# Kernel tuning notes

Measured on AMD Instinct MI355X. Metric: run time of the kernel, lower is better.

Reference implementation:

```python
import jax, jax.numpy as jnp
import numpy as np

D_MODEL = 1024
D_KV = 64
N_HEADS = 16
INNER = N_HEADS * D_KV
EPS = 1e-6


def setup_inputs() -> dict:
    key = jax.random.key(0)
    ks = jax.random.split(key, 8)
    B, SQ, SKV = 2, 2048, 4096
    hidden_states = jax.random.normal(ks[0], (B, SQ, D_MODEL), dtype=jnp.float32)
    key_value_states = jax.random.normal(ks[1], (B, SKV, D_MODEL), dtype=jnp.float32)
    attention_mask = jnp.zeros((B, 1, 1, SKV), dtype=jnp.float32)
    # nn.Linear(in, out, bias=False): y = x @ W.T; store W as [in, out] here
    s = 0.02
    Wq = jax.random.normal(ks[2], (D_MODEL, INNER), dtype=jnp.float32) * s
    Wk = jax.random.normal(ks[3], (D_MODEL, INNER), dtype=jnp.float32) * s
    Wv = jax.random.normal(ks[4], (D_MODEL, INNER), dtype=jnp.float32) * s
    Wo = jax.random.normal(ks[5], (INNER, D_MODEL), dtype=jnp.float32) * s
    ln_weight = jnp.ones((D_MODEL,), dtype=jnp.float32)
    return {
        "hidden_states": hidden_states,
        "key_value_states": key_value_states,
        "attention_mask": attention_mask,
        "ln_weight": ln_weight,
        "Wq": Wq,
        "Wk": Wk,
        "Wv": Wv,
        "Wo": Wo,
    }


def _t5_rmsnorm(x, w, eps=EPS):
    # no mean subtraction, variance in fp32
    var = jnp.mean(jnp.square(x.astype(jnp.float32)), axis=-1, keepdims=True)
    return w * (x * jax.lax.rsqrt(var + eps)).astype(x.dtype)


def reference(hidden_states, key_value_states, attention_mask, ln_weight, Wq, Wk, Wv, Wo):
    B, SQ, _ = hidden_states.shape
    SKV = key_value_states.shape[1]
    normed = _t5_rmsnorm(hidden_states, ln_weight)

    # projections -> [B, H, S, Dk]
    q = (normed @ Wq).reshape(B, SQ, N_HEADS, D_KV).transpose(0, 2, 1, 3)
    k = (key_value_states @ Wk).reshape(B, SKV, N_HEADS, D_KV).transpose(0, 2, 1, 3)
    v = (key_value_states @ Wv).reshape(B, SKV, N_HEADS, D_KV).transpose(0, 2, 1, 3)

    # T5: NO 1/sqrt(d) scaling
    scores = jnp.einsum("bhqd,bhkd->bhqk", q, k) + attention_mask
    attn = jax.nn.softmax(scores.astype(jnp.float32), axis=-1).astype(scores.dtype)
    ctx = jnp.einsum("bhqk,bhkd->bhqd", attn, v)
    ctx = ctx.transpose(0, 2, 1, 3).reshape(B, SQ, INNER)
    attn_out = ctx @ Wo
    return hidden_states + attn_out
```

## Files before the change

kernel.cpp:

```cpp
#include <hip/hip_runtime.h>

typedef unsigned short u16;
typedef unsigned int u32;
typedef __attribute__((ext_vector_type(4))) float f32x4;
typedef __attribute__((ext_vector_type(8))) short short8;
typedef __attribute__((ext_vector_type(4))) short short4v;

#define BB   2
#define SQL  2048
#define SKVL 4096
#define DM   1024
#define NH   16
#define DK   64
#define L2E  1.44269504f

#if __has_builtin(__builtin_amdgcn_exp2f)
#define EXP2(x) __builtin_amdgcn_exp2f(x)
#else
#define EXP2(x) exp2f(x)
#endif

#define MFMA32(a, b, c) __builtin_amdgcn_mfma_f32_16x16x32_bf16(a, b, c, 0, 0, 0)
#define MFMA16(a, b, c) __builtin_amdgcn_mfma_f32_16x16x16bf16_1k(a, b, c, 0, 0, 0)

__device__ __forceinline__ u16 f2bf(float f) {
  union { float f; unsigned u; } v; v.f = f;
  unsigned r = v.u + 0x7fff + ((v.u >> 16) & 1);
  return (u16)(r >> 16);
}

__device__ __forceinline__ short4v pack4(float p0, float p1, float p2, float p3) {
  union { float f; u32 u; } a, b, c, d;
  a.f = p0; b.f = p1; c.f = p2; d.f = p3;
  union { uint2 v; short4v s; } r;
  r.v.x = __builtin_amdgcn_perm(b.u + 0x8000u, a.u + 0x8000u, 0x07060302);
  r.v.y = __builtin_amdgcn_perm(d.u + 0x8000u, c.u + 0x8000u, 0x07060302);
  return r.s;
}

__device__ __forceinline__ void gload16(const void* g, void* lds) {
  __builtin_amdgcn_global_load_lds(
      (const __attribute__((address_space(1))) unsigned int*)g,
      (__attribute__((address_space(3))) unsigned int*)lds, 16, 0, 0);
}

__global__ void pre_kernel(const float* __restrict__ hidden, const float* __restrict__ lnw,
                           const float* __restrict__ kvs,
                           const float* __restrict__ Wq, const float* __restrict__ Wk,
                           const float* __restrict__ Wv, const float* __restrict__ Wo,
                           u16* __restrict__ normed, u16* __restrict__ kvb,
                           u16* __restrict__ Wqt, u16* __restrict__ Wkt,
                           u16* __restrict__ Wvt, u16* __restrict__ Wot) {
  __shared__ float red[4];
  __shared__ float tile[32][33];
  int bid = blockIdx.x, t = threadIdx.x;
  if (bid < 4096) {
    int row = bid;
    float4 v = ((const float4*)(hidden + (size_t)row * DM))[t];
    float ss = v.x * v.x + v.y * v.y + v.z * v.z + v.w * v.w;
#pragma unroll
    for (int m = 32; m >= 1; m >>= 1) ss += __shfl_xor(ss, m, 64);
    int lane = t & 63, wv = t >> 6;
    if (lane == 0) red[wv] = ss;
    __syncthreads();
    float total = red[0] + red[1] + red[2] + red[3];
    float scale = rsqrtf(total * (1.0f / DM) + 1e-6f);
    float4 g = ((const float4*)lnw)[t];
    ushort4 o;
    o.x = f2bf(v.x * scale * g.x);
    o.y = f2bf(v.y * scale * g.y);
    o.z = f2bf(v.z * scale * g.z);
    o.w = f2bf(v.w * scale * g.w);
    ((ushort4*)(normed + (size_t)row * DM))[t] = o;
  } else if (bid < 12288) {
    int i = (bid - 4096) * 256 + t;
    float4 v = ((const float4*)kvs)[i];
    ushort4 o;
    o.x = f2bf(v.x); o.y = f2bf(v.y); o.z = f2bf(v.z); o.w = f2bf(v.w);
    ((ushort4*)kvb)[i] = o;
  } else {
    int g = bid - 12288;
    int z = g >> 10;
    const float* W = (z == 0) ? Wq : (z == 1) ? Wk : (z == 2) ? Wv : Wo;
    u16* Wt = (z == 0) ? Wqt : (z == 1) ? Wkt : (z == 2) ? Wvt : Wot;
    int xx = g & 31, yy = (g >> 5) & 31;
    int tx = t & 31, ty = t >> 5;
    int k0 = yy * 32, n0 = xx * 32;
#pragma unroll
    for (int i = 0; i < 4; i++)
      tile[ty + i * 8][tx] = W[(size_t)(k0 + ty + i * 8) * DM + n0 + tx];
    __syncthreads();
#pragma unroll
    for (int i = 0; i < 4; i++)
      Wt[(size_t)(n0 + ty + i * 8) * DM + k0 + tx] = f2bf(tile[tx][ty + i * 8]);
  }
}

__global__ void proj_kernel(const u16* __restrict__ normed, const u16* __restrict__ kvb,
                            const u16* __restrict__ Wqt, const u16* __restrict__ Wkt,
                            const u16* __restrict__ Wvt,
                            u16* __restrict__ Qb, u16* __restrict__ Kbf,
                            u16* __restrict__ Vtb) {
  const int K = 1024;
  __shared__ __align__(16) u16 Al[128 * 32];
  __shared__ __align__(16) u16 Bl[128 * 32];
  int tid = threadIdx.x, lane = tid & 63, w = tid >> 6;
  int l15 = lane & 15, quad = lane >> 4;
  int wy = w >> 1, wx = w & 1;

  int bid = blockIdx.x;
  int mode;
  const u16 *A, *Bt;
  int tm, tn;
  if (bid < 256) { mode = 0; A = normed; Bt = Wqt; tm = (bid & 31) * 128; tn = (bid >> 5) * 128; }
  else if (bid < 768) { mode = 1; A = kvb; Bt = Wkt; int kid = bid - 256; tm = (kid & 63) * 128; tn = (kid >> 6) * 128; }
  else { mode = 2; A = Wvt; Bt = kvb; int vid = bid - 768; tm = (vid & 7) * 128; tn = (vid >> 3) * 128; }

  f32x4 acc[4][4] = {};
  for (int k0 = 0; k0 < K; k0 += 32) {
    __syncthreads();
#pragma unroll
    for (int r = 0; r < 2; r++) {
      int mg = w * 2 + r;
      gload16(A + (size_t)(tm + mg * 16 + l15) * K + k0 + quad * 8, &Al[mg * 512]);
      gload16(Bt + (size_t)(tn + mg * 16 + l15) * K + k0 + quad * 8, &Bl[mg * 512]);
    }
    __syncthreads();
    short8 af[4], bfr[4];
#pragma unroll
    for (int i = 0; i < 4; i++) {
      af[i] = *(const short8*)&Al[((wy * 4 + i) * 64 + lane) * 8];
      bfr[i] = *(const short8*)&Bl[((wx * 4 + i) * 64 + lane) * 8];
    }
#pragma unroll
    for (int mt = 0; mt < 4; mt++)
#pragma unroll
      for (int nt = 0; nt < 4; nt++)
        acc[mt][nt] = MFMA32(af[mt], bfr[nt], acc[mt][nt]);
  }

#pragma unroll
  for (int mt = 0; mt < 4; mt++) {
    int m0 = tm + wy * 64 + mt * 16 + quad * 4;
#pragma unroll
    for (int nt = 0; nt < 4; nt++) {
      int n = tn + wx * 64 + nt * 16 + l15;
      if (mode == 0) {
#pragma unroll
        for (int r = 0; r < 4; r++)
          Qb[(size_t)(m0 + r) * 1024 + n] = f2bf(acc[mt][nt][r] * L2E);
      } else if (mode == 1) {
#pragma unroll
        for (int r = 0; r < 4; r++)
          Kbf[(size_t)(m0 + r) * 1024 + n] = f2bf(acc[mt][nt][r]);
      } else {
        int b = n >> 12, skv = n & 4095;
        int kvt = skv >> 6, kvl = skv & 63;
        int p = kvl >> 5, kth = (kvl >> 4) & 1, qd = (kvl >> 2) & 3, elo = kvl & 3;
        int e = kth * 4 + elo;
        int h = m0 >> 6, d0 = m0 & 63;
        size_t base = ((size_t)((b * NH + h) * 64 + kvt) << 12) + (size_t)(p * 4 + qd) * 512 + e;
#pragma unroll
        for (int r = 0; r < 4; r++)
          Vtb[base + (size_t)(d0 + r) * 8] = f2bf(acc[mt][nt][r]);
      }
    }
  }
}

__global__ __launch_bounds__(256, 2) void flash_kernel(
    const u16* __restrict__ Qp, const u16* __restrict__ Kp, const u16* __restrict__ Vtb,
    const float* __restrict__ mask, u16* __restrict__ ctx) {
  __shared__ __align__(16) char smem[65536];
  u16* Kbuf = (u16*)smem;
  u16* Vbuf = (u16*)(smem + 32768);
  float* Ox = (float*)smem;
  float* Ll = (float*)(smem + 32768);

  int tid = threadIdx.x, lane = tid & 63, w = tid >> 6;
  int l15 = lane & 15, quad = lane >> 4;
  int grp = w >> 1, wg = w & 1;
  int qb = blockIdx.x, bh = blockIdx.y;
  int b = bh >> 4, h = bh & 15;
  int q0 = qb * 128 + wg * 64;

  short8 qf[4][2];
#pragma unroll
  for (int mt = 0; mt < 4; mt++)
#pragma unroll
    for (int kf = 0; kf < 2; kf++)
      qf[mt][kf] = *(const short8*)(Qp + (size_t)(b * SQL + q0 + mt * 16 + l15) * DM +
                                    h * DK + kf * 32 + quad * 8);

  f32x4 of[4][4] = {};
  f32x4 la[4] = {};
  const short4v ones = {0x3F80, 0x3F80, 0x3F80, 0x3F80};

  const size_t vblob = (size_t)(b * NH + h) * 64 * 4096;
  const float* mrow = mask + (size_t)b * SKVL;

  auto stage = [&](int tileIdx, int buf) {
    int kv0 = tileIdx * 64;
    u16* Kd = Kbuf + (buf * 2 + grp) * 4096;
    u16* Vd = Vbuf + (buf * 2 + grp) * 4096;
#pragma unroll
    for (int r = 0; r < 4; r++) {
      int u = wg * 4 + r;
      int kt = u >> 1, kf = u & 1;
      gload16(Kp + (size_t)(b * SKVL + kv0 + kt * 16 + l15) * DM + h * DK + kf * 32 + quad * 8,
              &Kd[u * 512]);
      gload16(Vtb + vblob + (size_t)tileIdx * 4096 + u * 512 + lane * 8, &Vd[u * 512]);
    }
  };

  f32x4 mlc[4], mln[4];
  {
    int kv0 = grp * 64;
#pragma unroll
    for (int kt = 0; kt < 4; kt++)
      mlc[kt] = *(const f32x4*)(mrow + kv0 + kt * 16 + quad * 4) * L2E;
  }
  stage(grp, 0);

  for (int it = 0; it < 32; ++it) {
    __syncthreads();
    if (it + 1 < 32) {
      stage((it + 1) * 2 + grp, (it + 1) & 1);
      int kvn = ((it + 1) * 2 + grp) * 64;
#pragma unroll
      for (int kt = 0; kt < 4; kt++)
        mln[kt] = *(const f32x4*)(mrow + kvn + kt * 16 + quad * 4) * L2E;
    }
    const u16* Kg = Kbuf + ((it & 1) * 2 + grp) * 4096;
    const u16* Vg = Vbuf + ((it & 1) * 2 + grp) * 4096;

#pragma unroll
    for (int ktp = 0; ktp < 2; ktp++) {
      short4v pa[2][4];
#pragma unroll
      for (int kth = 0; kth < 2; kth++) {
        int kt = ktp * 2 + kth;
        short8 k0 = *(const short8*)&Kg[((kt * 2 + 0) * 64 + lane) * 8];
        short8 k1 = *(const short8*)&Kg[((kt * 2 + 1) * 64 + lane) * 8];
#pragma unroll
        for (int mt = 0; mt < 4; mt++) {
          f32x4 st = mlc[kt];
          st = MFMA32(k0, qf[mt][0], st);
          st = MFMA32(k1, qf[mt][1], st);
          pa[kth][mt] = pack4(EXP2(st[0]), EXP2(st[1]), EXP2(st[2]), EXP2(st[3]));
        }
      }
#pragma unroll
      for (int mt = 0; mt < 4; mt++) {
        la[mt] = MFMA16(pa[0][mt], ones, la[mt]);
        la[mt] = MFMA16(pa[1][mt], ones, la[mt]);
      }
#pragma unroll
      for (int nt = 0; nt < 4; nt++) {
        short8 vv = *(const short8*)&Vg[((ktp * 4 + quad) * 64 + nt * 16 + l15) * 8];
        short4v vlo = {vv[0], vv[1], vv[2], vv[3]};
        short4v vhi = {vv[4], vv[5], vv[6], vv[7]};
#pragma unroll
        for (int mt = 0; mt < 4; mt++) {
          of[mt][nt] = MFMA16(pa[0][mt], vlo, of[mt][nt]);
          of[mt][nt] = MFMA16(pa[1][mt], vhi, of[mt][nt]);
        }
      }
    }
#pragma unroll
    for (int kt = 0; kt < 4; kt++) mlc[kt] = mln[kt];
  }

  __syncthreads();
  if (grp == 1) {
#pragma unroll
    for (int mt = 0; mt < 4; mt++) {
#pragma unroll
      for (int nt = 0; nt < 4; nt++)
#pragma unroll
        for (int r = 0; r < 4; r++)
          Ox[(wg * 64 + mt * 16 + quad * 4 + r) * 64 + nt * 16 + l15] = of[mt][nt][r];
      if (l15 == 0)
#pragma unroll
        for (int r = 0; r < 4; r++) Ll[wg * 64 + mt * 16 + quad * 4 + r] = la[mt][r];
    }
  }
  __syncthreads();
  if (grp == 0) {
#pragma unroll
    for (int mt = 0; mt < 4; mt++)
#pragma unroll
      for (int r = 0; r < 4; r++) {
        int ql = wg * 64 + mt * 16 + quad * 4 + r;
        float inv = 1.0f / (la[mt][r] + Ll[ql]);
        int q = qb * 128 + ql;
#pragma unroll
        for (int nt = 0; nt < 4; nt++) {
          float ov = of[mt][nt][r] + Ox[ql * 64 + nt * 16 + l15];
          ctx[(size_t)(b * SQL + q) * DM + h * DK + nt * 16 + l15] = f2bf(ov * inv);
        }
      }
  }
}

__global__ void ogemm_kernel(const u16* __restrict__ A, const u16* __restrict__ Bt,
                             float* __restrict__ C, const float* __restrict__ resid) {
  const int K = 1024;
  __shared__ __align__(16) u16 Al[128 * 32];
  __shared__ __align__(16) u16 Bl[128 * 32];
  int tid = threadIdx.x, lane = tid & 63, w = tid >> 6;
  int l15 = lane & 15, quad = lane >> 4;
  int wy = w >> 1, wx = w & 1;
  int tm = blockIdx.x * 128, tn = blockIdx.y * 128;
  f32x4 acc[4][4] = {};

  for (int k0 = 0; k0 < K; k0 += 32) {
    __syncthreads();
#pragma unroll
    for (int r = 0; r < 2; r++) {
      int mg = w * 2 + r;
      gload16(A + (size_t)(tm + mg * 16 + l15) * K + k0 + quad * 8, &Al[mg * 512]);
      gload16(Bt + (size_t)(tn + mg * 16 + l15) * K + k0 + quad * 8, &Bl[mg * 512]);
    }
    __syncthreads();
    short8 af[4], bfr[4];
#pragma unroll
    for (int i = 0; i < 4; i++) {
      af[i] = *(const short8*)&Al[((wy * 4 + i) * 64 + lane) * 8];
      bfr[i] = *(const short8*)&Bl[((wx * 4 + i) * 64 + lane) * 8];
    }
#pragma unroll
    for (int mt = 0; mt < 4; mt++)
#pragma unroll
      for (int nt = 0; nt < 4; nt++)
        acc[mt][nt] = MFMA32(af[mt], bfr[nt], acc[mt][nt]);
  }

#pragma unroll
  for (int mt = 0; mt < 4; mt++) {
    int m0 = tm + wy * 64 + mt * 16 + quad * 4;
#pragma unroll
    for (int nt = 0; nt < 4; nt++) {
      int n = tn + wx * 64 + nt * 16 + l15;
#pragma unroll
      for (int r = 0; r < 4; r++) {
        size_t idx = (size_t)(m0 + r) * 1024 + n;
        C[idx] = resid[idx] + acc[mt][nt][r];
      }
    }
  }
}

extern "C" void kernel_launch(void* const* d_in, const int* in_sizes, int n_in,
                              void* d_out, int out_size, void* d_ws, size_t ws_size,
                              hipStream_t stream) {
  const float* hidden = (const float*)d_in[0];
  const float* kvs    = (const float*)d_in[1];
  const float* mask   = (const float*)d_in[2];
  const float* lnw    = (const float*)d_in[3];
  const float* Wq     = (const float*)d_in[4];
  const float* Wk     = (const float*)d_in[5];
  const float* Wv     = (const float*)d_in[6];
  const float* Wo     = (const float*)d_in[7];
  char* ws = (char*)d_ws;

  u16* normed = (u16*)(ws + 0);
  u16* kvb    = (u16*)(ws + 8388608);
  u16* Wqt    = (u16*)(ws + 25165824);
  u16* Wkt    = (u16*)(ws + 27262976);
  u16* Wvt    = (u16*)(ws + 29360128);
  u16* Wot    = (u16*)(ws + 31457280);
  u16* Qb     = (u16*)(ws + 33554432);
  u16* Kbf    = (u16*)(ws + 41943040);
  u16* Vtb    = (u16*)(ws + 58720256);
  u16* ctxb   = (u16*)(ws + 75497472);

  pre_kernel<<<16384, 256, 0, stream>>>(hidden, lnw, kvs, Wq, Wk, Wv, Wo,
                                        normed, kvb, Wqt, Wkt, Wvt, Wot);
  proj_kernel<<<1280, 256, 0, stream>>>(normed, kvb, Wqt, Wkt, Wvt, Qb, Kbf, Vtb);
  flash_kernel<<<dim3(SQL / 128, BB * NH), 256, 0, stream>>>(Qb, Kbf, Vtb, mask, ctxb);
  ogemm_kernel<<<dim3(32, 8), 256, 0, stream>>>(ctxb, Wot, (float*)d_out, hidden);
}
```

Before: 324.1 us.

## Double-buffer GEMM LDS tiles and switch PV to 16x16x32 MFMA with new V layout

The projection and output GEMMs now stage the next K-slice into a second LDS buffer while computing on the current one, with one barrier per iteration instead of two. This is meant to hide global-load latency behind the MFMA work. The V projection output is re-laid out in 32-key groups so the flash kernel can feed P·V and the row-sum with single 16x16x32 bf16 MFMAs instead of pairs of 16x16x16. That halves the MFMA instruction count in the attention inner loop. The costs are double the LDS per GEMM block, and a correctness risk: the async LDS loads must have completed before the trailing barrier, and the new V layout must match exactly.

Result: slower. 337.8 us (+4.2%).

```diff
diff --git a/kernel.cpp b/kernel.cpp
--- a/kernel.cpp
+++ b/kernel.cpp
@@ -21,7 +21,6 @@
 #endif
 
 #define MFMA32(a, b, c) __builtin_amdgcn_mfma_f32_16x16x32_bf16(a, b, c, 0, 0, 0)
-#define MFMA16(a, b, c) __builtin_amdgcn_mfma_f32_16x16x16bf16_1k(a, b, c, 0, 0, 0)
 
 __device__ __forceinline__ u16 f2bf(float f) {
   union { float f; unsigned u; } v; v.f = f;
@@ -102,8 +101,8 @@
                             u16* __restrict__ Qb, u16* __restrict__ Kbf,
                             u16* __restrict__ Vtb) {
   const int K = 1024;
-  __shared__ __align__(16) u16 Al[128 * 32];
-  __shared__ __align__(16) u16 Bl[128 * 32];
+  __shared__ __align__(16) u16 Al[2][128 * 32];
+  __shared__ __align__(16) u16 Bl[2][128 * 32];
   int tid = threadIdx.x, lane = tid & 63, w = tid >> 6;
   int l15 = lane & 15, quad = lane >> 4;
   int wy = w >> 1, wx = w & 1;
@@ -116,27 +115,33 @@
   else if (bid < 768) { mode = 1; A = kvb; Bt = Wkt; int kid = bid - 256; tm = (kid & 63) * 128; tn = (kid >> 6) * 128; }
   else { mode = 2; A = Wvt; Bt = kvb; int vid = bid - 768; tm = (vid & 7) * 128; tn = (vid >> 3) * 128; }
 
-  f32x4 acc[4][4] = {};
-  for (int k0 = 0; k0 < K; k0 += 32) {
-    __syncthreads();
+  auto stage = [&](int k0, int buf) {
 #pragma unroll
     for (int r = 0; r < 2; r++) {
       int mg = w * 2 + r;
-      gload16(A + (size_t)(tm + mg * 16 + l15) * K + k0 + quad * 8, &Al[mg * 512]);
-      gload16(Bt + (size_t)(tn + mg * 16 + l15) * K + k0 + quad * 8, &Bl[mg * 512]);
-    }
-    __syncthreads();
+      gload16(A + (size_t)(tm + mg * 16 + l15) * K + k0 + quad * 8, &Al[buf][mg * 512]);
+      gload16(Bt + (size_t)(tn + mg * 16 + l15) * K + k0 + quad * 8, &Bl[buf][mg * 512]);
+    }
+  };
+
+  f32x4 acc[4][4] = {};
+  stage(0, 0);
+  __syncthreads();
+  for (int k0 = 0; k0 < K; k0 += 32) {
+    int cur = (k0 >> 5) & 1;
+    if (k0 + 32 < K) stage(k0 + 32, cur ^ 1);
     short8 af[4], bfr[4];
 #pragma unroll
     for (int i = 0; i < 4; i++) {
-      af[i] = *(const short8*)&Al[((wy * 4 + i) * 64 + lane) * 8];
-      bfr[i] = *(const short8*)&Bl[((wx * 4 + i) * 64 + lane) * 8];
+      af[i] = *(const short8*)&Al[cur][((wy * 4 + i) * 64 + lane) * 8];
+      bfr[i] = *(const short8*)&Bl[cur][((wx * 4 + i) * 64 + lane) * 8];
     }
 #pragma unroll
     for (int mt = 0; mt < 4; mt++)
 #pragma unroll
       for (int nt = 0; nt < 4; nt++)
         acc[mt][nt] = MFMA32(af[mt], bfr[nt], acc[mt][nt]);
+    __syncthreads();
   }
 
 #pragma unroll
@@ -155,14 +160,13 @@
           Kbf[(size_t)(m0 + r) * 1024 + n] = f2bf(acc[mt][nt][r]);
       } else {
         int b = n >> 12, skv = n & 4095;
-        int kvt = skv >> 6, kvl = skv & 63;
-        int p = kvl >> 5, kth = (kvl >> 4) & 1, qd = (kvl >> 2) & 3, elo = kvl & 3;
-        int e = kth * 4 + elo;
+        int t32 = skv >> 5, p = skv & 31;
+        int slot = ((p >> 2) & 3) * 8 + (p >> 4) * 4 + (p & 3);
         int h = m0 >> 6, d0 = m0 & 63;
-        size_t base = ((size_t)((b * NH + h) * 64 + kvt) << 12) + (size_t)(p * 4 + qd) * 512 + e;
+        size_t base = (size_t)((b * NH + h) * 128 + t32) * 2048 + (size_t)slot;
 #pragma unroll
         for (int r = 0; r < 4; r++)
-          Vtb[base + (size_t)(d0 + r) * 8] = f2bf(acc[mt][nt][r]);
+          Vtb[base + (size_t)(d0 + r) * 32] = f2bf(acc[mt][nt][r]);
       }
     }
   }
@@ -194,7 +198,7 @@
 
   f32x4 of[4][4] = {};
   f32x4 la[4] = {};
-  const short4v ones = {0x3F80, 0x3F80, 0x3F80, 0x3F80};
+  const short8 ones8 = {0x3F80, 0x3F80, 0x3F80, 0x3F80, 0x3F80, 0x3F80, 0x3F80, 0x3F80};
 
   const size_t vblob = (size_t)(b * NH + h) * 64 * 4096;
   const float* mrow = mask + (size_t)b * SKVL;
@@ -222,6 +226,8 @@
   }
   stage(grp, 0);
 
+  union PU { short8 v8; short4v h2[2]; };
+
   for (int it = 0; it < 32; ++it) {
     __syncthreads();
     if (it + 1 < 32) {
@@ -236,7 +242,7 @@
 
 #pragma unroll
     for (int ktp = 0; ktp < 2; ktp++) {
-      short4v pa[2][4];
+      PU paf[4];
 #pragma unroll
       for (int kth = 0; kth < 2; kth++) {
         int kt = ktp * 2 + kth;
@@ -247,24 +253,18 @@
           f32x4 st = mlc[kt];
           st = MFMA32(k0, qf[mt][0], st);
           st = MFMA32(k1, qf[mt][1], st);
-          pa[kth][mt] = pack4(EXP2(st[0]), EXP2(st[1]), EXP2(st[2]), EXP2(st[3]));
+          paf[mt].h2[kth] = pack4(EXP2(st[0]), EXP2(st[1]), EXP2(st[2]), EXP2(st[3]));
         }
       }
 #pragma unroll
-      for (int mt = 0; mt < 4; mt++) {
-        la[mt] = MFMA16(pa[0][mt], ones, la[mt]);
-        la[mt] = MFMA16(pa[1][mt], ones, la[mt]);
-      }
+      for (int mt = 0; mt < 4; mt++)
+        la[mt] = MFMA32(paf[mt].v8, ones8, la[mt]);
 #pragma unroll
       for (int nt = 0; nt < 4; nt++) {
-        short8 vv = *(const short8*)&Vg[((ktp * 4 + quad) * 64 + nt * 16 + l15) * 8];
-        short4v vlo = {vv[0], vv[1], vv[2], vv[3]};
-        short4v vhi = {vv[4], vv[5], vv[6], vv[7]};
-#pragma unroll
-        for (int mt = 0; mt < 4; mt++) {
-          of[mt][nt] = MFMA16(pa[0][mt], vlo, of[mt][nt]);
-          of[mt][nt] = MFMA16(pa[1][mt], vhi, of[mt][nt]);
-        }
+        short8 vv = *(const short8*)&Vg[ktp * 2048 + (nt * 16 + l15) * 32 + quad * 8];
+#pragma unroll
+        for (int mt = 0; mt < 4; mt++)
+          of[mt][nt] = MFMA32(paf[mt].v8, vv, of[mt][nt]);
       }
     }
 #pragma unroll
@@ -306,34 +306,40 @@
 __global__ void ogemm_kernel(const u16* __restrict__ A, const u16* __restrict__ Bt,
                              float* __restrict__ C, const float* __restrict__ resid) {
   const int K = 1024;
-  __shared__ __align__(16) u16 Al[128 * 32];
-  __shared__ __align__(16) u16 Bl[128 * 32];
+  __shared__ __align__(16) u16 Al[2][128 * 32];
+  __shared__ __align__(16) u16 Bl[2][128 * 32];
   int tid = threadIdx.x, lane = tid & 63, w = tid >> 6;
   int l15 = lane & 15, quad = lane >> 4;
   int wy = w >> 1, wx = w & 1;
   int tm = blockIdx.x * 128, tn = blockIdx.y * 128;
   f32x4 acc[4][4] = {};
 
-  for (int k0 = 0; k0 < K; k0 += 32) {
-    __syncthreads();
+  auto stage = [&](int k0, int buf) {
 #pragma unroll
     for (int r = 0; r < 2; r++) {
       int mg = w * 2 + r;
-      gload16(A + (size_t)(tm + mg * 16 + l15) * K + k0 + quad * 8, &Al[mg * 512]);
-      gload16(Bt + (size_t)(tn + mg * 16 + l15) * K + k0 + quad * 8, &Bl[mg * 512]);
-    }
-    __syncthreads();
+      gload16(A + (size_t)(tm + mg * 16 + l15) * K + k0 + quad * 8, &Al[buf][mg * 512]);
+      gload16(Bt + (size_t)(tn + mg * 16 + l15) * K + k0 + quad * 8, &Bl[buf][mg * 512]);
+    }
+  };
+
+  stage(0, 0);
+  __syncthreads();
+  for (int k0 = 0; k0 < K; k0 += 32) {
+    int cur = (k0 >> 5) & 1;
+    if (k0 + 32 < K) stage(k0 + 32, cur ^ 1);
     short8 af[4], bfr[4];
 #pragma unroll
     for (int i = 0; i < 4; i++) {
-      af[i] = *(const short8*)&Al[((wy * 4 + i) * 64 + lane) * 8];
-      bfr[i] = *(const short8*)&Bl[((wx * 4 + i) * 64 + lane) * 8];
+      af[i] = *(const short8*)&Al[cur][((wy * 4 + i) * 64 + lane) * 8];
+      bfr[i] = *(const short8*)&Bl[cur][((wx * 4 + i) * 64 + lane) * 8];
     }
 #pragma unroll
     for (int mt = 0; mt < 4; mt++)
 #pragma unroll
       for (int nt = 0; nt < 4; nt++)
         acc[mt][nt] = MFMA32(af[mt], bfr[nt], acc[mt][nt]);
+    __syncthreads();
   }
 
 #pragma unroll
```

## Restructure flash attention to 8 waves of 16 queries with K=32 PV MFMAs

Applied to the files above, without the earlier changes.

The flash kernel now launches 512 threads, and each of the 8 waves owns 16 query rows and walks all 64 KV tiles. This replaces the old scheme where two groups split the KV range and merged partial results through LDS at the end. The V layout written by the projection kernel is changed so that P·V and the row-sum can use the 16x16x32 bf16 MFMA instead of pairs of 16x16x16 ones, and the cross-group reduction is removed. In exchange, each wave now does less MFMA work per staged K/V tile, so the kernel may lean more on LDS reads and barriers. The change also depends on the new launch bounds giving higher occupancy.

Measured after the change: 347.0 us. 1.07x slower.

```diff
diff --git a/kernel.cpp b/kernel.cpp
--- a/kernel.cpp
+++ b/kernel.cpp
@@ -21,7 +21,6 @@
 #endif
 
 #define MFMA32(a, b, c) __builtin_amdgcn_mfma_f32_16x16x32_bf16(a, b, c, 0, 0, 0)
-#define MFMA16(a, b, c) __builtin_amdgcn_mfma_f32_16x16x16bf16_1k(a, b, c, 0, 0, 0)
 
 __device__ __forceinline__ u16 f2bf(float f) {
   union { float f; unsigned u; } v; v.f = f;
@@ -155,151 +154,103 @@
           Kbf[(size_t)(m0 + r) * 1024 + n] = f2bf(acc[mt][nt][r]);
       } else {
         int b = n >> 12, skv = n & 4095;
-        int kvt = skv >> 6, kvl = skv & 63;
-        int p = kvl >> 5, kth = (kvl >> 4) & 1, qd = (kvl >> 2) & 3, elo = kvl & 3;
-        int e = kth * 4 + elo;
+        int t32 = skv >> 5, p = skv & 31;
+        int s = ((p >> 2) & 3) * 8 + ((p >> 4) & 1) * 4 + (p & 3);
         int h = m0 >> 6, d0 = m0 & 63;
-        size_t base = ((size_t)((b * NH + h) * 64 + kvt) << 12) + (size_t)(p * 4 + qd) * 512 + e;
+        size_t base = (size_t)((b * NH + h) * 128 + t32) * 2048
+                    + (size_t)(d0 >> 4) * 512 + (size_t)(s >> 3) * 128 + (s & 7);
 #pragma unroll
         for (int r = 0; r < 4; r++)
-          Vtb[base + (size_t)(d0 + r) * 8] = f2bf(acc[mt][nt][r]);
+          Vtb[base + (size_t)((d0 & 15) + r) * 8] = f2bf(acc[mt][nt][r]);
       }
     }
   }
 }
 
-__global__ __launch_bounds__(256, 2) void flash_kernel(
+__global__ __launch_bounds__(512, 4) void flash_kernel(
     const u16* __restrict__ Qp, const u16* __restrict__ Kp, const u16* __restrict__ Vtb,
     const float* __restrict__ mask, u16* __restrict__ ctx) {
-  __shared__ __align__(16) char smem[65536];
-  u16* Kbuf = (u16*)smem;
-  u16* Vbuf = (u16*)(smem + 32768);
-  float* Ox = (float*)smem;
-  float* Ll = (float*)(smem + 32768);
+  __shared__ __align__(16) u16 Kbuf[2][4096];
+  __shared__ __align__(16) u16 Vbuf[2][4096];
 
   int tid = threadIdx.x, lane = tid & 63, w = tid >> 6;
   int l15 = lane & 15, quad = lane >> 4;
-  int grp = w >> 1, wg = w & 1;
   int qb = blockIdx.x, bh = blockIdx.y;
   int b = bh >> 4, h = bh & 15;
-  int q0 = qb * 128 + wg * 64;
-
-  short8 qf[4][2];
-#pragma unroll
-  for (int mt = 0; mt < 4; mt++)
-#pragma unroll
-    for (int kf = 0; kf < 2; kf++)
-      qf[mt][kf] = *(const short8*)(Qp + (size_t)(b * SQL + q0 + mt * 16 + l15) * DM +
-                                    h * DK + kf * 32 + quad * 8);
-
-  f32x4 of[4][4] = {};
-  f32x4 la[4] = {};
-  const short4v ones = {0x3F80, 0x3F80, 0x3F80, 0x3F80};
-
-  const size_t vblob = (size_t)(b * NH + h) * 64 * 4096;
+  int q0 = qb * 128 + w * 16;
+
+  short8 qf[2];
+#pragma unroll
+  for (int kf = 0; kf < 2; kf++)
+    qf[kf] = *(const short8*)(Qp + (size_t)(b * SQL + q0 + l15) * DM +
+                              h * DK + kf * 32 + quad * 8);
+
+  f32x4 of[4] = {};
+  f32x4 la = {};
+  const short8 ones8 = {0x3F80, 0x3F80, 0x3F80, 0x3F80, 0x3F80, 0x3F80, 0x3F80, 0x3F80};
+
+  const size_t vblob = (size_t)(b * NH + h) * 262144;
   const float* mrow = mask + (size_t)b * SKVL;
 
-  auto stage = [&](int tileIdx, int buf) {
-    int kv0 = tileIdx * 64;
-    u16* Kd = Kbuf + (buf * 2 + grp) * 4096;
-    u16* Vd = Vbuf + (buf * 2 + grp) * 4096;
-#pragma unroll
-    for (int r = 0; r < 4; r++) {
-      int u = wg * 4 + r;
-      int kt = u >> 1, kf = u & 1;
-      gload16(Kp + (size_t)(b * SKVL + kv0 + kt * 16 + l15) * DM + h * DK + kf * 32 + quad * 8,
-              &Kd[u * 512]);
-      gload16(Vtb + vblob + (size_t)tileIdx * 4096 + u * 512 + lane * 8, &Vd[u * 512]);
-    }
+  auto stage = [&](int t, int buf) {
+    int kv0 = t * 64;
+    int kt = w >> 1, kf = w & 1;
+    gload16(Kp + (size_t)(b * SKVL + kv0 + kt * 16 + l15) * DM + h * DK + kf * 32 + quad * 8,
+            &Kbuf[buf][w * 512]);
+    gload16(Vtb + vblob + (size_t)t * 4096 + w * 512 + lane * 8, &Vbuf[buf][w * 512]);
   };
 
   f32x4 mlc[4], mln[4];
-  {
-    int kv0 = grp * 64;
-#pragma unroll
-    for (int kt = 0; kt < 4; kt++)
-      mlc[kt] = *(const f32x4*)(mrow + kv0 + kt * 16 + quad * 4) * L2E;
-  }
-  stage(grp, 0);
-
-  for (int it = 0; it < 32; ++it) {
-    __syncthreads();
-    if (it + 1 < 32) {
-      stage((it + 1) * 2 + grp, (it + 1) & 1);
-      int kvn = ((it + 1) * 2 + grp) * 64;
+#pragma unroll
+  for (int kt = 0; kt < 4; kt++)
+    mlc[kt] = *(const f32x4*)(mrow + kt * 16 + quad * 4) * L2E;
+  stage(0, 0);
+
+  union PU { short8 v8; short4v h2[2]; };
+
+  for (int it = 0; it < 64; ++it) {
+    __syncthreads();
+    if (it + 1 < 64) {
+      stage(it + 1, (it + 1) & 1);
+      int kvn = (it + 1) * 64;
 #pragma unroll
       for (int kt = 0; kt < 4; kt++)
         mln[kt] = *(const f32x4*)(mrow + kvn + kt * 16 + quad * 4) * L2E;
     }
-    const u16* Kg = Kbuf + ((it & 1) * 2 + grp) * 4096;
-    const u16* Vg = Vbuf + ((it & 1) * 2 + grp) * 4096;
+    const u16* Kg = Kbuf[it & 1];
+    const u16* Vg = Vbuf[it & 1];
 
 #pragma unroll
     for (int ktp = 0; ktp < 2; ktp++) {
-      short4v pa[2][4];
+      PU pa;
 #pragma unroll
       for (int kth = 0; kth < 2; kth++) {
         int kt = ktp * 2 + kth;
         short8 k0 = *(const short8*)&Kg[((kt * 2 + 0) * 64 + lane) * 8];
         short8 k1 = *(const short8*)&Kg[((kt * 2 + 1) * 64 + lane) * 8];
-#pragma unroll
-        for (int mt = 0; mt < 4; mt++) {
-          f32x4 st = mlc[kt];
-          st = MFMA32(k0, qf[mt][0], st);
-          st = MFMA32(k1, qf[mt][1], st);
-          pa[kth][mt] = pack4(EXP2(st[0]), EXP2(st[1]), EXP2(st[2]), EXP2(st[3]));
-        }
+        f32x4 st = mlc[kt];
+        st = MFMA32(k0, qf[0], st);
+        st = MFMA32(k1, qf[1], st);
+        pa.h2[kth] = pack4(EXP2(st[0]), EXP2(st[1]), EXP2(st[2]), EXP2(st[3]));
       }
-#pragma unroll
-      for (int mt = 0; mt < 4; mt++) {
-        la[mt] = MFMA16(pa[0][mt], ones, la[mt]);
-        la[mt] = MFMA16(pa[1][mt], ones, la[mt]);
+      la = MFMA32(pa.v8, ones8, la);
+#pragma unroll
+      for (int nt = 0; nt < 4; nt++) {
+        short8 vv = *(const short8*)&Vg[ktp * 2048 + (nt * 64 + lane) * 8];
+        of[nt] = MFMA32(pa.v8, vv, of[nt]);
       }
-#pragma unroll
-      for (int nt = 0; nt < 4; nt++) {
-        short8 vv = *(const short8*)&Vg[((ktp * 4 + quad) * 64 + nt * 16 + l15) * 8];
-        short4v vlo = {vv[0], vv[1], vv[2], vv[3]};
-        short4v vhi = {vv[4], vv[5], vv[6], vv[7]};
-#pragma unroll
-        for (int mt = 0; mt < 4; mt++) {
-          of[mt][nt] = MFMA16(pa[0][mt], vlo, of[mt][nt]);
-          of[mt][nt] = MFMA16(pa[1][mt], vhi, of[mt][nt]);
-        }
-      }
     }
 #pragma unroll
     for (int kt = 0; kt < 4; kt++) mlc[kt] = mln[kt];
   }
 
-  __syncthreads();
-  if (grp == 1) {
-#pragma unroll
-    for (int mt = 0; mt < 4; mt++) {
-#pragma unroll
-      for (int nt = 0; nt < 4; nt++)
-#pragma unroll
-        for (int r = 0; r < 4; r++)
-          Ox[(wg * 64 + mt * 16 + quad * 4 + r) * 64 + nt * 16 + l15] = of[mt][nt][r];
-      if (l15 == 0)
-#pragma unroll
-        for (int r = 0; r < 4; r++) Ll[wg * 64 + mt * 16 + quad * 4 + r] = la[mt][r];
-    }
-  }
-  __syncthreads();
-  if (grp == 0) {
-#pragma unroll
-    for (int mt = 0; mt < 4; mt++)
-#pragma unroll
-      for (int r = 0; r < 4; r++) {
-        int ql = wg * 64 + mt * 16 + quad * 4 + r;
-        float inv = 1.0f / (la[mt][r] + Ll[ql]);
-        int q = qb * 128 + ql;
-#pragma unroll
-        for (int nt = 0; nt < 4; nt++) {
-          float ov = of[mt][nt][r] + Ox[ql * 64 + nt * 16 + l15];
-          ctx[(size_t)(b * SQL + q) * DM + h * DK + nt * 16 + l15] = f2bf(ov * inv);
-        }
-      }
+#pragma unroll
+  for (int r = 0; r < 4; r++) {
+    int q = q0 + quad * 4 + r;
+    float inv = 1.0f / la[r];
+#pragma unroll
+    for (int nt = 0; nt < 4; nt++)
+      ctx[(size_t)(b * SQL + q) * DM + h * DK + nt * 16 + l15] = f2bf(of[nt][r] * inv);
   }
 }
 
@@ -378,6 +329,6 @@
   pre_kernel<<<16384, 256, 0, stream>>>(hidden, lnw, kvs, Wq, Wk, Wv, Wo,
                                         normed, kvb, Wqt, Wkt, Wvt, Wot);
   proj_kernel<<<1280, 256, 0, stream>>>(normed, kvb, Wqt, Wkt, Wvt, Qb, Kbf, Vtb);
-  flash_kernel<<<dim3(SQL / 128, BB * NH), 256, 0, stream>>>(Qb, Kbf, Vtb, mask, ctxb);
+  flash_kernel<<<dim3(SQL / 128, BB * NH), 512, 0, stream>>>(Qb, Kbf, Vtb, mask, ctxb);
   ogemm_kernel<<<dim3(32, 8), 256, 0, stream>>>(ctxb, Wot, (float*)d_out, hidden);
 }
```

## Use 16x16x32 MFMA for PV and rowsum with re-laid V tiles; XCD-aware block remap

Applied to the files above, without the earlier changes.

Changes the V-transpose layout produced by the projection kernel so each lane can feed a single 16x16x32 bf16 MFMA. The P·V product and the softmax row-sum now use one MFMA instead of two 16x16x16 MFMAs, which removes the V register unpacking and halves the instruction count for that stage. It also remaps block IDs so blocks that share a (batch, head) land on the same XCD, aiming to improve L2 reuse of K and V. The risk is that the new V layout, the packed P fragment and the block mapping must all line up exactly with the MFMA operand ordering.

Result: no change. 323.6 us (-0.1%).

```diff
diff --git a/kernel.cpp b/kernel.cpp
--- a/kernel.cpp
+++ b/kernel.cpp
@@ -21,7 +21,6 @@
 #endif
 
 #define MFMA32(a, b, c) __builtin_amdgcn_mfma_f32_16x16x32_bf16(a, b, c, 0, 0, 0)
-#define MFMA16(a, b, c) __builtin_amdgcn_mfma_f32_16x16x16bf16_1k(a, b, c, 0, 0, 0)
 
 __device__ __forceinline__ u16 f2bf(float f) {
   union { float f; unsigned u; } v; v.f = f;
@@ -155,14 +154,14 @@
           Kbf[(size_t)(m0 + r) * 1024 + n] = f2bf(acc[mt][nt][r]);
       } else {
         int b = n >> 12, skv = n & 4095;
-        int kvt = skv >> 6, kvl = skv & 63;
-        int p = kvl >> 5, kth = (kvl >> 4) & 1, qd = (kvl >> 2) & 3, elo = kvl & 3;
-        int e = kth * 4 + elo;
+        int t32 = skv >> 5, p = skv & 31;
+        int s = ((p >> 2) & 3) * 8 + ((p >> 4) & 1) * 4 + (p & 3);
         int h = m0 >> 6, d0 = m0 & 63;
-        size_t base = ((size_t)((b * NH + h) * 64 + kvt) << 12) + (size_t)(p * 4 + qd) * 512 + e;
+        size_t base = (size_t)((b * NH + h) * 128 + t32) * 2048
+                    + (size_t)(d0 >> 4) * 512 + (size_t)(s >> 3) * 128 + (s & 7);
 #pragma unroll
         for (int r = 0; r < 4; r++)
-          Vtb[base + (size_t)(d0 + r) * 8] = f2bf(acc[mt][nt][r]);
+          Vtb[base + (size_t)((d0 & 15) + r) * 8] = f2bf(acc[mt][nt][r]);
       }
     }
   }
@@ -180,7 +179,11 @@
   int tid = threadIdx.x, lane = tid & 63, w = tid >> 6;
   int l15 = lane & 15, quad = lane >> 4;
   int grp = w >> 1, wg = w & 1;
-  int qb = blockIdx.x, bh = blockIdx.y;
+
+  int lid = blockIdx.y * 16 + blockIdx.x;
+  int xcd = lid & 7, slot = lid >> 3;
+  int bh = xcd * 4 + (slot >> 4);
+  int qb = slot & 15;
   int b = bh >> 4, h = bh & 15;
   int q0 = qb * 128 + wg * 64;
 
@@ -194,9 +197,9 @@
 
   f32x4 of[4][4] = {};
   f32x4 la[4] = {};
-  const short4v ones = {0x3F80, 0x3F80, 0x3F80, 0x3F80};
-
-  const size_t vblob = (size_t)(b * NH + h) * 64 * 4096;
+  const short8 ones8 = {0x3F80, 0x3F80, 0x3F80, 0x3F80, 0x3F80, 0x3F80, 0x3F80, 0x3F80};
+
+  const size_t vblob = (size_t)(b * NH + h) * 262144;
   const float* mrow = mask + (size_t)b * SKVL;
 
   auto stage = [&](int tileIdx, int buf) {
@@ -222,6 +225,8 @@
   }
   stage(grp, 0);
 
+  union PU { short8 v8; short4v h2[2]; };
+
   for (int it = 0; it < 32; ++it) {
     __syncthreads();
     if (it + 1 < 32) {
@@ -236,7 +241,7 @@
 
 #pragma unroll
     for (int ktp = 0; ktp < 2; ktp++) {
-      short4v pa[2][4];
+      PU paf[4];
 #pragma unroll
       for (int kth = 0; kth < 2; kth++) {
         int kt = ktp * 2 + kth;
@@ -247,24 +252,18 @@
           f32x4 st = mlc[kt];
           st = MFMA32(k0, qf[mt][0], st);
           st = MFMA32(k1, qf[mt][1], st);
-          pa[kth][mt] = pack4(EXP2(st[0]), EXP2(st[1]), EXP2(st[2]), EXP2(st[3]));
+          paf[mt].h2[kth] = pack4(EXP2(st[0]), EXP2(st[1]), EXP2(st[2]), EXP2(st[3]));
         }
       }
 #pragma unroll
-      for (int mt = 0; mt < 4; mt++) {
-        la[mt] = MFMA16(pa[0][mt], ones, la[mt]);
-        la[mt] = MFMA16(pa[1][mt], ones, la[mt]);
-      }
+      for (int mt = 0; mt < 4; mt++)
+        la[mt] = MFMA32(paf[mt].v8, ones8, la[mt]);
 #pragma unroll
       for (int nt = 0; nt < 4; nt++) {
-        short8 vv = *(const short8*)&Vg[((ktp * 4 + quad) * 64 + nt * 16 + l15) * 8];
-        short4v vlo = {vv[0], vv[1], vv[2], vv[3]};
-        short4v vhi = {vv[4], vv[5], vv[6], vv[7]};
-#pragma unroll
-        for (int mt = 0; mt < 4; mt++) {
-          of[mt][nt] = MFMA16(pa[0][mt], vlo, of[mt][nt]);
-          of[mt][nt] = MFMA16(pa[1][mt], vhi, of[mt][nt]);
-        }
+        short8 vv = *(const short8*)&Vg[ktp * 2048 + (nt * 64 + lane) * 8];
+#pragma unroll
+        for (int mt = 0; mt < 4; mt++)
+          of[mt][nt] = MFMA32(paf[mt].v8, vv, of[mt][nt]);
       }
     }
 #pragma unroll
```
